# Optimization experiments

Hardware: AMD Instinct MI355X
Metric: run time of the kernel (lower is better)

## Reference

```python
import jax, jax.numpy as jnp
from jax import lax
import numpy as np

V, E, NF = 50000, 300, 1          # vocab, embed_size, n_features
H = 256                            # hidden size (both layers)
B, TH, TB = 128, 32, 512           # batch, headline len, body len
NC = 4                             # n_classes


def setup_inputs() -> dict:
    key = jax.random.key(0)
    ks = jax.random.split(key, 24)
    emb = jax.random.normal(ks[0], (V, E), jnp.float32) * 0.1
    emb = emb.at[0].set(0.0)  # pad token -> zero row so seqlen masking is meaningful

    def make_ids(kid, klen, T):
        raw = jax.random.randint(kid, (B, T, NF), 1, V)
        lens = jax.random.randint(klen, (B,), max(T // 4, 1), T + 1)
        mask = jnp.arange(T)[None, :, None] < lens[:, None, None]
        return jnp.where(mask, raw, 0)

    headline_ids = make_ids(ks[1], ks[2], TH)
    body_ids = make_ids(ks[3], ks[4], TB)

    def gru_params(k, din, h):
        k1, k2 = jax.random.split(k, 2)
        s = 1.0 / np.sqrt(din + h)
        return (jax.random.normal(k1, (din + h, 2 * h), jnp.float32) * s,
                jnp.ones((2 * h,), jnp.float32),          # TF GRUCell gate bias init = 1.0
                jax.random.normal(k2, (din + h, h), jnp.float32) * s,
                jnp.zeros((h,), jnp.float32))

    D0 = NF * E
    hd0 = gru_params(ks[5], D0, H)
    hd1 = gru_params(ks[6], H, H)
    bd0 = gru_params(ks[7], D0, H)
    bd1 = gru_params(ks[8], H, H)

    W_pred = jax.random.normal(ks[9], (2 * H, NC), jnp.float32) * (1.0 / np.sqrt(2 * H))
    b_pred = jnp.zeros((NC,), jnp.float32)

    out = {"headline_ids": headline_ids, "body_ids": body_ids, "embeddings": emb,
           "W_pred": W_pred, "b_pred": b_pred}
    for pref, p in (("hd0", hd0), ("hd1", hd1), ("bd0", bd0), ("bd1", bd1)):
        out[pref + "_Wg"], out[pref + "_bg"], out[pref + "_Wc"], out[pref + "_bc"] = p
    return out


def _seq_length(x):
    # used = sign(max(|x|, axis=2)); seqlen = sum over time
    return jnp.sum(jnp.sign(jnp.max(jnp.abs(x), axis=2)), axis=1).astype(jnp.int32)


def _gru_layer(x, seqlen, Wg, bg, Wc, bc):
    # x: [B, T, D] -> outputs [B, T, H], final state [B, H]; dynamic_rnn semantics:
    # past seqlen, output is zero and state is copied through.
    Bsz, T, _ = x.shape
    Hh = Wc.shape[1]
    xt = jnp.swapaxes(x, 0, 1)  # [T, B, D]
    tids = jnp.arange(T)

    def step(h, inp):
        xi, t = inp
        xh = jnp.concatenate([xi, h], axis=-1)
        r, u = jnp.split(jax.nn.sigmoid(xh @ Wg + bg), 2, axis=-1)
        c = jnp.tanh(jnp.concatenate([xi, r * h], axis=-1) @ Wc + bc)
        nh = u * h + (1.0 - u) * c
        valid = (t < seqlen)[:, None]
        out = jnp.where(valid, nh, 0.0)
        h_next = jnp.where(valid, nh, h)
        return h_next, out

    h0 = jnp.zeros((Bsz, Hh), x.dtype)
    hf, outs = lax.scan(step, h0, (xt, tids))
    return jnp.swapaxes(outs, 0, 1), hf


def _stream(ids, emb, layers):
    x = emb[ids].reshape(ids.shape[0], ids.shape[1], -1)  # [B, T, NF*E]
    h = None
    for (Wg, bg, Wc, bc) in layers:
        sl = _seq_length(x)  # recomputed from current layer inputs, as in the source
        x, h = _gru_layer(x, sl, Wg, bg, Wc, bc)
    return h


def reference(headline_ids, body_ids, embeddings,
              hd0_Wg, hd0_bg, hd0_Wc, hd0_bc, hd1_Wg, hd1_bg, hd1_Wc, hd1_bc,
              bd0_Wg, bd0_bg, bd0_Wc, bd0_bc, bd1_Wg, bd1_bg, bd1_Wc, bd1_bc,
              W_pred, b_pred):
    h_head = _stream(headline_ids, embeddings,
                     [(hd0_Wg, hd0_bg, hd0_Wc, hd0_bc), (hd1_Wg, hd1_bg, hd1_Wc, hd1_bc)])
    h_body = _stream(body_ids, embeddings,
                     [(bd0_Wg, bd0_bg, bd0_Wc, bd0_bc), (bd1_Wg, bd1_bg, bd1_Wc, bd1_bc)])
    pred_input = jnp.concatenate([h_head, h_body], axis=1)  # [B, 2H]
    return pred_input @ W_pred + b_pred                      # [B, NC]
```

## Files before the change

### kernel.cpp

```cpp
#include <hip/hip_runtime.h>
#include <cstdint>
#include <cstddef>

#define H_    256
#define NG    768
#define BATCH 128
#define TH_   32
#define TB_   512
#define E_    300
#define RPB   16
#define CH_   16
#define NCH   32
#define NT_   192
#define RING  4
#define NJ    72
#define NGRU  24
#define NWORK 200
#define GRID  (NGRU + NWORK)

#define G0S   ((size_t)BATCH * CH_ * NG)
#define OCS   ((size_t)BATCH * CH_ * H_)

#define F_QHEAD 0
#define F_CNT0  1
#define F_CNT1  33
#define F_L0F   65
#define F_L1F   97
#define F_HCNT0 129
#define F_HCNT1 131
#define F_HL0F  133
#define F_NUM   136

typedef _Float16 half8 __attribute__((ext_vector_type(8)));
typedef _Float16 half4 __attribute__((ext_vector_type(4)));
typedef float    floatx4 __attribute__((ext_vector_type(4)));

#define AS1 __attribute__((address_space(1)))
#define AS3 __attribute__((address_space(3)))

#define WC_LGKM0 0xC07F
#define WCVM(N)  (0x0F70 | ((N) & 15) | (((N) >> 4) << 14))

__global__ __launch_bounds__(256) void pack_bias(
    const float* __restrict__ bg, const float* __restrict__ bc,
    float* __restrict__ bias)
{
  int idx = blockIdx.x * 256 + threadIdx.x;
  if (idx < NG) bias[idx] = (idx < 2 * H_) ? bg[idx] : bc[idx - 2 * H_];
}

__global__ __launch_bounds__(256) void pack_bx(
    const float* __restrict__ Wg, const float* __restrict__ Wc,
    int din, int KT, _Float16* __restrict__ out)
{
  int idx = blockIdx.x * 256 + threadIdx.x;
  if (idx >= KT * 48 * 64) return;
  int lane = idx & 63, tile = idx >> 6;
  int kt = tile / 48, nt = tile - kt * 48;
  int col = nt * 16 + (lane & 15);
  int k0 = kt * 32 + (lane >> 4) * 8;
  const float* W; int ncols, c2;
  if (col < 2 * H_) { W = Wg; ncols = 2 * H_; c2 = col; }
  else              { W = Wc; ncols = H_;     c2 = col - 2 * H_; }
  _Float16* dst = out + ((size_t)(kt * 48 + nt) * 64 + lane) * 8;
#pragma unroll
  for (int j = 0; j < 8; ++j) {
    int k = k0 + j;
    dst[j] = (k < din) ? (_Float16)W[(size_t)k * ncols + c2] : (_Float16)0.f;
  }
}

__global__ __launch_bounds__(256) void pack_w(
    const float* __restrict__ Wg, const float* __restrict__ Wc, int din,
    _Float16* __restrict__ wpk)
{
  int idx = blockIdx.x * 256 + threadIdx.x;
  if (idx >= 48 * 64) return;
  int tile = idx >> 6, lane = idx & 63;
  int grp = tile >> 4, tt = tile & 15;
  int wv = tt >> 1, s = tt & 1;
  const float* W; int ncols, n0;
  if (grp == 0)      { W = Wg; ncols = 2 * H_; n0 = wv * 32 + s * 16; }
  else if (grp == 1) { W = Wg; ncols = 2 * H_; n0 = 256 + wv * 32 + s * 16; }
  else               { W = Wc; ncols = H_;     n0 = wv * 32 + s * 16; }
  int n = n0 + (lane & 15);
  int kb = (lane >> 4) * 8;
#pragma unroll
  for (int kt = 0; kt < 8; ++kt) {
    _Float16* dst = wpk + ((size_t)(tile * 8 + kt) * 64 + lane) * 8;
#pragma unroll
    for (int j = 0; j < 8; ++j)
      dst[j] = (_Float16)W[(size_t)(din + kt * 32 + kb + j) * ncols + n];
  }
}

__global__ __launch_bounds__(256) void seq_k(const int* __restrict__ ids, int T,
                                             int* __restrict__ seq)
{
  __shared__ int red[256];
  int b = blockIdx.x, tid = threadIdx.x;
  int cnt = 0;
  for (int t = tid; t < T; t += 256) cnt += (ids[b * T + t] != 0) ? 1 : 0;
  red[tid] = cnt;
  __syncthreads();
  for (int s = 128; s > 0; s >>= 1) {
    if (tid < s) red[tid] += red[tid + s];
    __syncthreads();
  }
  if (tid == 0) seq[b] = red[0];
}

struct GemmJob {
  const _Float16* Adir; const int* ids; const _Float16* Bpk;
  const float* bias; _Float16* G;
  int K; int KT; int t0; int tcsh; int T;
};

struct PArgs {
  const float* emb; const int* idsH; const int* idsB;
  const int* seqH; const int* seqB;
  const _Float16 *Wpk0, *Wpk1, *Wpk2, *Wpk3;
  const _Float16 *Bx0, *Bx1, *Bx2, *Bx3;
  const float *bi0, *bi1, *bi2, *bi3;
  _Float16 *G0r, *G1r, *Ocr;
  _Float16 *GH0, *GH1, *OcH;
  float *hfH, *hfB;
  int* flg;
};

union SMem {
  struct { _Float16 hpk[4096]; _Float16 rpk[4096]; _Float16 Gs[4][12288]; } g;
  struct { _Float16 Al[2][64 * 40]; _Float16 Bl[2][8 * 512]; } m;
  int bcast;
};

__device__ __forceinline__ void gemm_block(const GemmJob& jb, const float* emb,
                                           int lb, SMem& sm)
{
  auto& Al = sm.m.Al;
  auto& Bl = sm.m.Bl;
  const int tid = threadIdx.x;
  const int w = tid >> 6, lane = tid & 63;
  const int quad = lane >> 4, l15 = lane & 15;
  const int gx = lb / 6, gy = lb - gx * 6;
  const int m0 = gx * 64, n0 = gy * 128;
  const int K = jb.K, KT = jb.KT, tcsh = jb.tcsh;
  const int tc = 1 << tcsh;

  const int am = tid >> 3, ak = tid & 7;
  const int arow = m0 + am;
  const _Float16* asrch = nullptr;
  const float*    asrcf = nullptr;
  if (jb.Adir) {
    asrch = jb.Adir + (size_t)arow * K;
  } else {
    int b = arow >> tcsh, tl = arow & (tc - 1);
    asrcf = emb + (size_t)jb.ids[b * jb.T + jb.t0 + tl] * K;
  }

  float a4[4];
  auto loadA = [&](int kt) {
    int k0 = kt * 32 + ak * 4;
    if (asrch) {
      half4 hv = *(const half4*)&asrch[k0];
#pragma unroll
      for (int j = 0; j < 4; ++j) a4[j] = (float)hv[j];
    } else {
#pragma unroll
      for (int j = 0; j < 4; ++j) a4[j] = (k0 + j < K) ? asrcf[k0 + j] : 0.f;
    }
  };
  auto writeA = [&](int buf) {
    half4 v;
#pragma unroll
    for (int j = 0; j < 4; ++j) v[j] = (_Float16)a4[j];
    *(half4*)&Al[buf][am * 40 + ak * 4] = v;
  };
  auto stageB = [&](int kt, int buf) {
    int nt = (n0 >> 4) + w;
    const _Float16* src = jb.Bpk + ((size_t)(kt * 48 + nt) * 64 + lane) * 8;
    __builtin_amdgcn_global_load_lds(
        (const AS1 unsigned int*)src,
        (AS3 unsigned int*)&Bl[buf][w * 512 + lane * 8], 16, 0, 0);
  };

  loadA(0);
  stageB(0, 0);
  writeA(0);
  floatx4 acc[4] = {};

  for (int kt = 0; kt < KT; ++kt) {
    const int buf = kt & 1;
    __syncthreads();
    if (kt + 1 < KT) { loadA(kt + 1); stageB(kt + 1, buf ^ 1); }
    half8 bf = *(const half8*)&Bl[buf][w * 512 + lane * 8];
#pragma unroll
    for (int st = 0; st < 4; ++st) {
      half8 af = *(const half8*)&Al[buf][(st * 16 + l15) * 40 + quad * 8];
      acc[st] = __builtin_amdgcn_mfma_f32_16x16x32_f16(af, bf, acc[st], 0, 0, 0);
    }
    if (kt + 1 < KT) writeA(buf ^ 1);
  }

  int col = n0 + w * 16 + l15;
  float bb = jb.bias[col];
  int g = col >> 8, kk = col & 255;
  int ww = kk >> 5, ss = (kk >> 4) & 1, ll = kk & 15;
  int cc = 2 * g + ss;
#pragma unroll
  for (int st = 0; st < 4; ++st) {
#pragma unroll
    for (int r = 0; r < 4; ++r) {
      int grow = m0 + st * 16 + quad * 4 + r;
      int b = grow >> tcsh, tl = grow & (tc - 1);
      int rg = b >> 4, mm = b & 15, qb = mm >> 2, rb = mm & 3;
      jb.G[((size_t)tl * BATCH + rg * RPB) * NG +
           ((ww * 6 + cc) * 64 + qb * 16 + ll) * 4 + rb] =
          (_Float16)(acc[st][r] + bb);
    }
  }
}

struct GruRun {
  const _Float16* W; const int* seq; int rg; int nch;
  const _Float16* Gb; size_t gs; int ring;
  _Float16* Ob; size_t os;
  float* stOut;
  int* wflag; int wtar;
  int* w2flag;
  int* pflag;
};

__device__ __forceinline__ void gru_run(const GruRun& P, SMem& sm)
{
  _Float16* hpk = sm.g.hpk;
  _Float16* rpk = sm.g.rpk;
  auto& Gs = sm.g.Gs;

  const int tid = threadIdx.x;
  const int w = tid >> 6, lane = tid & 63;
  const int quad = lane >> 4, l15 = lane & 15;

  floatx4 wg[4][8];
  floatx4 wc[2][8];
#pragma unroll
  for (int i = 0; i < 4; ++i) {
    const int tile = (i >> 1) * 16 + w * 2 + (i & 1);
#pragma unroll
    for (int kt = 0; kt < 8; ++kt) {
      wg[i][kt] = *(const floatx4*)&P.W[((size_t)(tile * 8 + kt) * 64 + lane) * 8];
      asm volatile("" : "+v"(wg[i][kt]));
    }
  }
#pragma unroll
  for (int i = 0; i < 2; ++i) {
    const int tile = 32 + w * 2 + i;
#pragma unroll
    for (int kt = 0; kt < 8; ++kt) {
      wc[i][kt] = *(const floatx4*)&P.W[((size_t)(tile * 8 + kt) * 64 + lane) * 8];
      asm volatile("" : "+a"(wc[i][kt]));
    }
  }

  int seq4[4];
#pragma unroll
  for (int r = 0; r < 4; ++r) seq4[r] = P.seq[P.rg * RPB + quad * 4 + r];
  int Smax = 0;
#pragma unroll
  for (int i = 0; i < 16; ++i) Smax = max(Smax, P.seq[P.rg * RPB + i]);

  const int wbase = (w * 64 + quad * 2 + (l15 >> 3)) * 8 + (l15 & 7);
  const int rbase = (((quad >> 1) << 5) + ((l15 & 3) << 3) +
                     ((l15 >> 2) << 1) + (quad & 1)) * 8;

  float h_reg[2][4];
#pragma unroll
  for (int s = 0; s < 2; ++s)
#pragma unroll
    for (int r = 0; r < 4; ++r) {
      h_reg[s][r] = 0.f;
      hpk[wbase + s * 256 + r * 64] = (_Float16)0.f;
    }

  const _Float16* hA = &hpk[rbase];
  const _Float16* rA = &rpk[rbase];

  for (int c = 0; c < P.nch; ++c) {
    if (tid == 0) {
      while (__hip_atomic_load(&P.wflag[c], __ATOMIC_RELAXED,
                               __HIP_MEMORY_SCOPE_AGENT) < P.wtar)
        __builtin_amdgcn_s_sleep(2);
      if (P.w2flag && c >= RING)
        while (__hip_atomic_load(&P.w2flag[c - RING], __ATOMIC_RELAXED,
                                 __HIP_MEMORY_SCOPE_AGENT) < NT_)
          __builtin_amdgcn_s_sleep(2);
      __builtin_amdgcn_fence(__ATOMIC_ACQUIRE, "agent");
    }
    __syncthreads();

    const int slot = P.ring ? (c & (RING - 1)) : c;
    const _Float16* G = P.Gb + (size_t)slot * P.gs;
    _Float16* outp = P.Ob ? P.Ob + (size_t)slot * P.os : nullptr;
    const int t0 = c * CH_;
    int steps = Smax - t0;
    if (steps < 0) steps = 0;
    if (steps > CH_) steps = CH_;

    const _Float16* gblk = G + (size_t)P.rg * RPB * NG + w * 1536;
    _Float16* ldsw = &Gs[0][0] + w * 1536;
    auto stage = [&](int t, int buf) {
      const _Float16* gp = gblk + (size_t)t * BATCH * NG;
      _Float16* lp = ldsw + buf * 12288;
#pragma unroll
      for (int i = 0; i < 3; ++i) {
        __builtin_amdgcn_global_load_lds(
            (const AS1 unsigned int*)(gp + i * 512 + lane * 8),
            (AS3 unsigned int*)(lp + i * 512), 16, 0, 0);
      }
    };
    if (steps > 0) stage(0, 0);
    __syncthreads();
    if (steps > 1) stage(1, 1);
    if (steps > 2) stage(2, 2);

    for (int t = 0; t < steps; ++t) {
      const int buf = t & 3;
      if (t + 3 < steps) stage(t + 3, (t + 3) & 3);

      floatx4 acc[4] = {};
#pragma unroll
      for (int kt = 0; kt < 8; ++kt) {
        half8 a = *(const half8*)&hA[kt * 512];
#pragma unroll
        for (int s = 0; s < 4; ++s)
          acc[s] = __builtin_amdgcn_mfma_f32_16x16x32_f16(
              a, __builtin_bit_cast(half8, wg[s][kt]), acc[s], 0, 0, 0);
      }

      {
        int np = outp ? ((t < 3) ? t : 3) : 0;
        int nf = steps - 1 - t; if (nf > 3) nf = 3;
        switch (np * 4 + nf) {
          case  0: __builtin_amdgcn_s_waitcnt(WCVM(0));  break;
          case  1: __builtin_amdgcn_s_waitcnt(WCVM(3));  break;
          case  2: __builtin_amdgcn_s_waitcnt(WCVM(6));  break;
          case  3: __builtin_amdgcn_s_waitcnt(WCVM(9));  break;
          case  4: __builtin_amdgcn_s_waitcnt(WCVM(8));  break;
          case  5: __builtin_amdgcn_s_waitcnt(WCVM(11)); break;
          case  6: __builtin_amdgcn_s_waitcnt(WCVM(14)); break;
          case  7: __builtin_amdgcn_s_waitcnt(WCVM(17)); break;
          case  8: __builtin_amdgcn_s_waitcnt(WCVM(16)); break;
          case  9: __builtin_amdgcn_s_waitcnt(WCVM(19)); break;
          case 10: __builtin_amdgcn_s_waitcnt(WCVM(22)); break;
          case 11: __builtin_amdgcn_s_waitcnt(WCVM(25)); break;
          case 12: __builtin_amdgcn_s_waitcnt(WCVM(24)); break;
          case 13: __builtin_amdgcn_s_waitcnt(WCVM(27)); break;
          case 14: __builtin_amdgcn_s_waitcnt(WCVM(30)); break;
          default: __builtin_amdgcn_s_waitcnt(WCVM(33)); break;
        }
      }

      floatx4 gA[4];
#pragma unroll
      for (int cc = 0; cc < 4; ++cc) {
        half4 hv = *(const half4*)&Gs[buf][(w * 6 + cc) * 256 + lane * 4];
#pragma unroll
        for (int j = 0; j < 4; ++j) gA[cc][j] = (float)hv[j];
      }

#pragma unroll
      for (int s = 0; s < 2; ++s)
#pragma unroll
        for (int r = 0; r < 4; ++r) {
          float pre = acc[s][r] + gA[s][r];
          float g = __builtin_amdgcn_rcpf(1.f + __expf(-pre));
          rpk[wbase + s * 256 + r * 64] = (_Float16)(g * h_reg[s][r]);
        }
      float u_reg[2][4];
#pragma unroll
      for (int s = 0; s < 2; ++s)
#pragma unroll
        for (int r = 0; r < 4; ++r) {
          float pre = acc[2 + s][r] + gA[2 + s][r];
          u_reg[s][r] = __builtin_amdgcn_rcpf(1.f + __expf(-pre));
        }
      __builtin_amdgcn_s_waitcnt(WC_LGKM0);
      __builtin_amdgcn_s_barrier();

      floatx4 accB[2] = {};
#pragma unroll
      for (int kt = 0; kt < 8; ++kt) {
        half8 a = *(const half8*)&rA[kt * 512];
#pragma unroll
        for (int s = 0; s < 2; ++s)
          accB[s] = __builtin_amdgcn_mfma_f32_16x16x32_f16(
              a, __builtin_bit_cast(half8, wc[s][kt]), accB[s], 0, 0, 0);
      }
      floatx4 gB[2];
#pragma unroll
      for (int s = 0; s < 2; ++s) {
        half4 hv = *(const half4*)&Gs[buf][(w * 6 + 4 + s) * 256 + lane * 4];
#pragma unroll
        for (int j = 0; j < 4; ++j) gB[s][j] = (float)hv[j];
      }

#pragma unroll
      for (int s = 0; s < 2; ++s)
#pragma unroll
        for (int r = 0; r < 4; ++r) {
          int row = quad * 4 + r;
          float pre = accB[s][r] + gB[s][r];
          float cv = 1.f - 2.f * __builtin_amdgcn_rcpf(1.f + __expf(2.f * pre));
          float u = u_reg[s][r];
          float hn = u * h_reg[s][r] + (1.f - u) * cv;
          bool valid = (t0 + t) < seq4[r];
          hn = valid ? hn : h_reg[s][r];
          h_reg[s][r] = hn;
          hpk[wbase + s * 256 + r * 64] = (_Float16)hn;
          if (outp)
            outp[((size_t)(P.rg * RPB + row) * CH_ + t) * H_ +
                 (w * 32 + s * 16 + l15)] = (_Float16)(valid ? hn : 0.f);
        }
      __builtin_amdgcn_s_waitcnt(WC_LGKM0);
      __builtin_amdgcn_s_barrier();
    }

    __syncthreads();
    if (P.pflag && tid == 0) {
      __builtin_amdgcn_fence(__ATOMIC_RELEASE, "agent");
      __hip_atomic_fetch_add(&P.pflag[c], 1, __ATOMIC_RELAXED,
                             __HIP_MEMORY_SCOPE_AGENT);
    }
  }

  if (P.stOut) {
#pragma unroll
    for (int s = 0; s < 2; ++s)
#pragma unroll
      for (int r = 0; r < 4; ++r)
        P.stOut[(size_t)(P.rg * RPB + quad * 4 + r) * H_ +
                (w * 32 + s * 16 + l15)] = h_reg[s][r];
  }
}

__device__ __forceinline__ void worker(const PArgs& a, SMem& sm)
{
  int* flg = a.flg;
  for (;;) {
    if (threadIdx.x == 0)
      sm.bcast = __hip_atomic_fetch_add(&flg[F_QHEAD], 1, __ATOMIC_RELAXED,
                                        __HIP_MEMORY_SCOPE_AGENT);
    __syncthreads();
    int tile = sm.bcast;
    __syncthreads();
    if (tile >= NJ * NT_) return;
    int q = tile / NT_, lb = tile - q * NT_;

    GemmJob jb{};
    int* post = nullptr;
    int* d1 = nullptr; int d1t = 0;
    int* d2 = nullptr; int d2t = 0;
    bool skip = false;

    if (q < 4) {
      int c = q;
      jb = {nullptr, a.idsB, a.Bx2, a.bi2, a.G0r + (size_t)(c & 3) * G0S,
            E_, 10, c * CH_, 4, TB_};
      post = &flg[F_CNT0 + c];
    } else if (q < 6) {
      int c = q - 4;
      jb = {nullptr, a.idsH, a.Bx0, a.bi0, a.GH0 + (size_t)c * G0S,
            E_, 10, c * CH_, 4, TH_};
      post = &flg[F_HCNT0 + c];
    } else if (q < 8) {
      int c = q - 6;
      jb = {a.OcH + (size_t)c * OCS, nullptr, a.Bx1, a.bi1,
            a.GH1 + (size_t)c * G0S, H_, 8, 0, 4, TH_};
      d1 = &flg[F_HL0F + c]; d1t = 8;
      post = &flg[F_HCNT1 + c];
    } else {
      int k = (q - 8) >> 1;
      if (((q - 8) & 1) == 0) {
        jb = {a.Ocr + (size_t)(k & 3) * OCS, nullptr, a.Bx3, a.bi3,
              a.G1r + (size_t)(k & 3) * G0S, H_, 8, 0, 4, TB_};
        d1 = &flg[F_L0F + k]; d1t = 8;
        if (k >= RING) { d2 = &flg[F_L1F + (k - RING)]; d2t = 8; }
        post = &flg[F_CNT1 + k];
      } else {
        int c = k + 4;
        if (c >= NCH) skip = true;
        else {
          jb = {nullptr, a.idsB, a.Bx2, a.bi2, a.G0r + (size_t)(c & 3) * G0S,
                E_, 10, c * CH_, 4, TB_};
          d1 = &flg[F_L0F + (c - RING)]; d1t = 8;
          post = &flg[F_CNT0 + c];
        }
      }
    }
    if (skip) continue;

    if (threadIdx.x == 0) {
      if (d1)
        while (__hip_atomic_load(d1, __ATOMIC_RELAXED,
                                 __HIP_MEMORY_SCOPE_AGENT) < d1t)
          __builtin_amdgcn_s_sleep(8);
      if (d2)
        while (__hip_atomic_load(d2, __ATOMIC_RELAXED,
                                 __HIP_MEMORY_SCOPE_AGENT) < d2t)
          __builtin_amdgcn_s_sleep(8);
      __builtin_amdgcn_fence(__ATOMIC_ACQUIRE, "agent");
    }
    __syncthreads();

    gemm_block(jb, a.emb, lb, sm);

    __syncthreads();
    if (threadIdx.x == 0) {
      __builtin_amdgcn_fence(__ATOMIC_RELEASE, "agent");
      __hip_atomic_fetch_add(post, 1, __ATOMIC_RELAXED,
                             __HIP_MEMORY_SCOPE_AGENT);
    }
  }
}

__global__ __launch_bounds__(512, 1) void pers(PArgs a)
{
  __shared__ SMem sm;
  const int bid = blockIdx.x;
  int* flg = a.flg;

  if (bid < 8) {
    GruRun P{a.Wpk2, a.seqB, bid, NCH, a.G0r, G0S, 1,
             a.Ocr, OCS, nullptr,
             &flg[F_CNT0], NT_, &flg[F_CNT1], &flg[F_L0F]};
    gru_run(P, sm);
  } else if (bid < 16) {
    GruRun P{a.Wpk3, a.seqB, bid - 8, NCH, a.G1r, G0S, 1,
             nullptr, 0, a.hfB,
             &flg[F_CNT1], NT_, nullptr, &flg[F_L1F]};
    gru_run(P, sm);
  } else if (bid < NGRU) {
    GruRun P0{a.Wpk0, a.seqH, bid - 16, 2, a.GH0, G0S, 0,
              a.OcH, OCS, nullptr,
              &flg[F_HCNT0], NT_, nullptr, &flg[F_HL0F]};
    gru_run(P0, sm);
    GruRun P1{a.Wpk1, a.seqH, bid - 16, 2, a.GH1, G0S, 0,
              nullptr, 0, a.hfH,
              &flg[F_HCNT1], NT_, nullptr, nullptr};
    gru_run(P1, sm);
  } else {
    worker(a, sm);
  }
}

__global__ __launch_bounds__(512) void pred_k(
    const float* __restrict__ hh, const float* __restrict__ hb,
    const float* __restrict__ Wp, const float* __restrict__ bpred,
    float* __restrict__ out)
{
  int tid = threadIdx.x;
  int b = tid >> 2, c = tid & 3;
  float acc = bpred[c];
  for (int k = 0; k < H_; ++k) acc += hh[b * H_ + k] * Wp[k * 4 + c];
  for (int k = 0; k < H_; ++k) acc += hb[b * H_ + k] * Wp[(H_ + k) * 4 + c];
  out[b * 4 + c] = acc;
}

extern "C" void kernel_launch(void* const* d_in, const int* in_sizes, int n_in,
                              void* d_out, int out_size, void* d_ws, size_t ws_size,
                              hipStream_t stream)
{
  (void)in_sizes; (void)n_in; (void)out_size; (void)ws_size;
  const int*   idsH = (const int*)  d_in[0];
  const int*   idsB = (const int*)  d_in[1];
  const float* emb  = (const float*)d_in[2];
  const float* Wp   = (const float*)d_in[3];
  const float* bp   = (const float*)d_in[4];
  const float* W[4][4];
  for (int s = 0; s < 4; ++s)
    for (int q = 0; q < 4; ++q)
      W[s][q] = (const float*)d_in[5 + s * 4 + q];

  float* wbase = (float*)d_ws;
  size_t off = 0;
  auto alloc = [&](size_t n) {
    float* p = wbase + off; off += (n + 255) & ~(size_t)255; return p;
  };

  int* flg = (int*)alloc(F_NUM);
  int* seqH = (int*)alloc(BATCH);
  int* seqB = (int*)alloc(BATCH);
  float* bi[4]; _Float16* Wpk[4]; _Float16* Bxh[4];
  const int din[4] = {E_, H_, E_, H_};
  const int KT[4]  = {10, 8, 10, 8};
  for (int s = 0; s < 4; ++s) {
    bi[s]  = alloc(NG);
    Wpk[s] = (_Float16*)alloc(48 * 8 * 64 * 8 / 2);
    Bxh[s] = (_Float16*)alloc((size_t)KT[s] * 48 * 64 * 8 / 2);
  }
  float* hfH = alloc((size_t)BATCH * H_);
  float* hfB = alloc((size_t)BATCH * H_);

  _Float16* GH0 = (_Float16*)alloc(2 * G0S / 2);
  _Float16* GH1 = (_Float16*)alloc(2 * G0S / 2);
  _Float16* OcH = (_Float16*)alloc(2 * OCS / 2);
  _Float16* G0r = (_Float16*)alloc(RING * G0S / 2);
  _Float16* G1r = (_Float16*)alloc(RING * G0S / 2);
  _Float16* Ocr = (_Float16*)alloc(RING * OCS / 2);

  hipMemsetAsync(flg, 0, F_NUM * sizeof(int), stream);

  for (int s = 0; s < 4; ++s) {
    pack_bias<<<(NG + 255) / 256, 256, 0, stream>>>(W[s][1], W[s][3], bi[s]);
    pack_w<<<(48 * 64 + 255) / 256, 256, 0, stream>>>(
        W[s][0], W[s][2], din[s], Wpk[s]);
    pack_bx<<<(KT[s] * 48 * 64 + 255) / 256, 256, 0, stream>>>(
        W[s][0], W[s][2], din[s], KT[s], Bxh[s]);
  }
  seq_k<<<BATCH, 256, 0, stream>>>(idsH, TH_, seqH);
  seq_k<<<BATCH, 256, 0, stream>>>(idsB, TB_, seqB);

  PArgs a;
  a.emb = emb; a.idsH = idsH; a.idsB = idsB; a.seqH = seqH; a.seqB = seqB;
  a.Wpk0 = Wpk[0]; a.Wpk1 = Wpk[1]; a.Wpk2 = Wpk[2]; a.Wpk3 = Wpk[3];
  a.Bx0 = Bxh[0]; a.Bx1 = Bxh[1]; a.Bx2 = Bxh[2]; a.Bx3 = Bxh[3];
  a.bi0 = bi[0]; a.bi1 = bi[1]; a.bi2 = bi[2]; a.bi3 = bi[3];
  a.G0r = G0r; a.G1r = G1r; a.Ocr = Ocr;
  a.GH0 = GH0; a.GH1 = GH1; a.OcH = OcH;
  a.hfH = hfH; a.hfB = hfB; a.flg = flg;
  pers<<<GRID, 512, 0, stream>>>(a);

  pred_k<<<1, 512, 0, stream>>>(hfH, hfB, Wp, bp, (float*)d_out);
}
```

Measured before the change: 2.213 ms.

## Use per-row-group dependency flags and restructure GRU step MFMA scheduling

Replaces the per-chunk global counters with per-chunk, per-row-group flags, so each GRU block waits only on the 24 GEMM tiles covering its own 16 batch rows instead of all 192. Pipelines can then advance per row group rather than per whole chunk. The GRU step is also reordered: G-tile reads are hoisted before the next prefetch, gate MFMAs are split so the reset-gate math overlaps the update-gate MFMAs, and the candidate matmul uses split-K accumulators. Per-step validity selects are replaced by a snapshot of the final state at seqlen, which changes the padded-step output semantics. This relies on padded steps being harmless given zero pad embeddings and zero inputs past seqlen.

```diff
diff --git a/kernel.cpp b/kernel.cpp
--- a/kernel.cpp
+++ b/kernel.cpp
@@ -12,6 +12,7 @@
 #define CH_   16
 #define NCH   32
 #define NT_   192
+#define NTRG  24
 #define RING  4
 #define NJ    72
 #define NGRU  24
@@ -23,13 +24,13 @@
 
 #define F_QHEAD 0
 #define F_CNT0  1
-#define F_CNT1  33
-#define F_L0F   65
-#define F_L1F   97
-#define F_HCNT0 129
-#define F_HCNT1 131
-#define F_HL0F  133
-#define F_NUM   136
+#define F_L0F   257
+#define F_CNT1  513
+#define F_L1F   769
+#define F_HCNT0 1025
+#define F_HL0F  1041
+#define F_HCNT1 1057
+#define F_NUM   1073
 
 typedef _Float16 half8 __attribute__((ext_vector_type(8)));
 typedef _Float16 half4 __attribute__((ext_vector_type(4)));
@@ -273,12 +274,13 @@
   const int rbase = (((quad >> 1) << 5) + ((l15 & 3) << 3) +
                      ((l15 >> 2) << 1) + (quad & 1)) * 8;
 
-  float h_reg[2][4];
+  const bool dosnap = (P.stOut != nullptr);
+  float h_reg[2][4], snap[2][4];
 #pragma unroll
   for (int s = 0; s < 2; ++s)
 #pragma unroll
     for (int r = 0; r < 4; ++r) {
-      h_reg[s][r] = 0.f;
+      h_reg[s][r] = 0.f; snap[s][r] = 0.f;
       hpk[wbase + s * 256 + r * 64] = (_Float16)0.f;
     }
 
@@ -287,12 +289,13 @@
 
   for (int c = 0; c < P.nch; ++c) {
     if (tid == 0) {
-      while (__hip_atomic_load(&P.wflag[c], __ATOMIC_RELAXED,
+      while (__hip_atomic_load(&P.wflag[c * 8 + P.rg], __ATOMIC_RELAXED,
                                __HIP_MEMORY_SCOPE_AGENT) < P.wtar)
         __builtin_amdgcn_s_sleep(2);
       if (P.w2flag && c >= RING)
-        while (__hip_atomic_load(&P.w2flag[c - RING], __ATOMIC_RELAXED,
-                                 __HIP_MEMORY_SCOPE_AGENT) < NT_)
+        while (__hip_atomic_load(&P.w2flag[(c - RING) * 8 + P.rg],
+                                 __ATOMIC_RELAXED,
+                                 __HIP_MEMORY_SCOPE_AGENT) < NTRG)
           __builtin_amdgcn_s_sleep(2);
       __builtin_amdgcn_fence(__ATOMIC_ACQUIRE, "agent");
     }
@@ -325,102 +328,116 @@
 
     for (int t = 0; t < steps; ++t) {
       const int buf = t & 3;
-      if (t + 3 < steps) stage(t + 3, (t + 3) & 3);
-
-      floatx4 acc[4] = {};
-#pragma unroll
-      for (int kt = 0; kt < 8; ++kt) {
-        half8 a = *(const half8*)&hA[kt * 512];
-#pragma unroll
-        for (int s = 0; s < 4; ++s)
-          acc[s] = __builtin_amdgcn_mfma_f32_16x16x32_f16(
-              a, __builtin_bit_cast(half8, wg[s][kt]), acc[s], 0, 0, 0);
-      }
 
       {
         int np = outp ? ((t < 3) ? t : 3) : 0;
-        int nf = steps - 1 - t; if (nf > 3) nf = 3;
-        switch (np * 4 + nf) {
+        int nf = steps - 1 - t; if (nf > 2) nf = 2;
+        switch (np * 3 + nf) {
           case  0: __builtin_amdgcn_s_waitcnt(WCVM(0));  break;
           case  1: __builtin_amdgcn_s_waitcnt(WCVM(3));  break;
           case  2: __builtin_amdgcn_s_waitcnt(WCVM(6));  break;
-          case  3: __builtin_amdgcn_s_waitcnt(WCVM(9));  break;
-          case  4: __builtin_amdgcn_s_waitcnt(WCVM(8));  break;
-          case  5: __builtin_amdgcn_s_waitcnt(WCVM(11)); break;
-          case  6: __builtin_amdgcn_s_waitcnt(WCVM(14)); break;
-          case  7: __builtin_amdgcn_s_waitcnt(WCVM(17)); break;
-          case  8: __builtin_amdgcn_s_waitcnt(WCVM(16)); break;
-          case  9: __builtin_amdgcn_s_waitcnt(WCVM(19)); break;
-          case 10: __builtin_amdgcn_s_waitcnt(WCVM(22)); break;
-          case 11: __builtin_amdgcn_s_waitcnt(WCVM(25)); break;
-          case 12: __builtin_amdgcn_s_waitcnt(WCVM(24)); break;
-          case 13: __builtin_amdgcn_s_waitcnt(WCVM(27)); break;
-          case 14: __builtin_amdgcn_s_waitcnt(WCVM(30)); break;
-          default: __builtin_amdgcn_s_waitcnt(WCVM(33)); break;
+          case  3: __builtin_amdgcn_s_waitcnt(WCVM(8));  break;
+          case  4: __builtin_amdgcn_s_waitcnt(WCVM(11)); break;
+          case  5: __builtin_amdgcn_s_waitcnt(WCVM(14)); break;
+          case  6: __builtin_amdgcn_s_waitcnt(WCVM(16)); break;
+          case  7: __builtin_amdgcn_s_waitcnt(WCVM(19)); break;
+          case  8: __builtin_amdgcn_s_waitcnt(WCVM(22)); break;
+          case  9: __builtin_amdgcn_s_waitcnt(WCVM(24)); break;
+          case 10: __builtin_amdgcn_s_waitcnt(WCVM(27)); break;
+          default: __builtin_amdgcn_s_waitcnt(WCVM(30)); break;
         }
       }
 
-      floatx4 gA[4];
-#pragma unroll
-      for (int cc = 0; cc < 4; ++cc) {
-        half4 hv = *(const half4*)&Gs[buf][(w * 6 + cc) * 256 + lane * 4];
-#pragma unroll
-        for (int j = 0; j < 4; ++j) gA[cc][j] = (float)hv[j];
-      }
-
-#pragma unroll
-      for (int s = 0; s < 2; ++s)
-#pragma unroll
-        for (int r = 0; r < 4; ++r) {
-          float pre = acc[s][r] + gA[s][r];
-          float g = __builtin_amdgcn_rcpf(1.f + __expf(-pre));
-          rpk[wbase + s * 256 + r * 64] = (_Float16)(g * h_reg[s][r]);
-        }
-      float u_reg[2][4];
-#pragma unroll
-      for (int s = 0; s < 2; ++s)
-#pragma unroll
-        for (int r = 0; r < 4; ++r) {
-          float pre = acc[2 + s][r] + gA[2 + s][r];
-          u_reg[s][r] = __builtin_amdgcn_rcpf(1.f + __expf(-pre));
-        }
+      half4 hga[6];
+#pragma unroll
+      for (int cc = 0; cc < 6; ++cc)
+        hga[cc] = *(const half4*)&Gs[buf][(w * 6 + cc) * 256 + lane * 4];
+
+      if (t + 3 < steps) stage(t + 3, (t + 3) & 3);
+
+      floatx4 a0 = {}, a1 = {};
+#pragma unroll
+      for (int kt = 0; kt < 8; ++kt) {
+        half8 a = *(const half8*)&hA[kt * 512];
+        a0 = __builtin_amdgcn_mfma_f32_16x16x32_f16(
+            a, __builtin_bit_cast(half8, wg[0][kt]), a0, 0, 0, 0);
+        a1 = __builtin_amdgcn_mfma_f32_16x16x32_f16(
+            a, __builtin_bit_cast(half8, wg[1][kt]), a1, 0, 0, 0);
+      }
+#pragma unroll
+      for (int r = 0; r < 4; ++r) {
+        float pre0 = a0[r] + (float)hga[0][r];
+        float g0 = __builtin_amdgcn_rcpf(1.f + __expf(-pre0));
+        rpk[wbase + 0 * 256 + r * 64] = (_Float16)(g0 * h_reg[0][r]);
+        float pre1 = a1[r] + (float)hga[1][r];
+        float g1 = __builtin_amdgcn_rcpf(1.f + __expf(-pre1));
+        rpk[wbase + 1 * 256 + r * 64] = (_Float16)(g1 * h_reg[1][r]);
+      }
+      floatx4 a2 = {}, a3 = {};
+#pragma unroll
+      for (int kt = 0; kt < 8; ++kt) {
+        half8 a = *(const half8*)&hA[kt * 512];
+        a2 = __builtin_amdgcn_mfma_f32_16x16x32_f16(
+            a, __builtin_bit_cast(half8, wg[2][kt]), a2, 0, 0, 0);
+        a3 = __builtin_amdgcn_mfma_f32_16x16x32_f16(
+            a, __builtin_bit_cast(half8, wg[3][kt]), a3, 0, 0, 0);
+      }
       __builtin_amdgcn_s_waitcnt(WC_LGKM0);
       __builtin_amdgcn_s_barrier();
 
-      floatx4 accB[2] = {};
-#pragma unroll
-      for (int kt = 0; kt < 8; ++kt) {
+      floatx4 c0 = {}, c1 = {}, c2 = {}, c3 = {};
+#pragma unroll
+      for (int kt = 0; kt < 4; ++kt) {
         half8 a = *(const half8*)&rA[kt * 512];
-#pragma unroll
-        for (int s = 0; s < 2; ++s)
-          accB[s] = __builtin_amdgcn_mfma_f32_16x16x32_f16(
-              a, __builtin_bit_cast(half8, wc[s][kt]), accB[s], 0, 0, 0);
-      }
-      floatx4 gB[2];
-#pragma unroll
-      for (int s = 0; s < 2; ++s) {
-        half4 hv = *(const half4*)&Gs[buf][(w * 6 + 4 + s) * 256 + lane * 4];
-#pragma unroll
-        for (int j = 0; j < 4; ++j) gB[s][j] = (float)hv[j];
+        c0 = __builtin_amdgcn_mfma_f32_16x16x32_f16(
+            a, __builtin_bit_cast(half8, wc[0][kt]), c0, 0, 0, 0);
+        c2 = __builtin_amdgcn_mfma_f32_16x16x32_f16(
+            a, __builtin_bit_cast(half8, wc[1][kt]), c2, 0, 0, 0);
+      }
+#pragma unroll
+      for (int kt = 4; kt < 8; ++kt) {
+        half8 a = *(const half8*)&rA[kt * 512];
+        c1 = __builtin_amdgcn_mfma_f32_16x16x32_f16(
+            a, __builtin_bit_cast(half8, wc[0][kt]), c1, 0, 0, 0);
+        c3 = __builtin_amdgcn_mfma_f32_16x16x32_f16(
+            a, __builtin_bit_cast(half8, wc[1][kt]), c3, 0, 0, 0);
+      }
+      float u_reg[2][4];
+#pragma unroll
+      for (int r = 0; r < 4; ++r) {
+        u_reg[0][r] = __builtin_amdgcn_rcpf(
+            1.f + __expf(-(a2[r] + (float)hga[2][r])));
+        u_reg[1][r] = __builtin_amdgcn_rcpf(
+            1.f + __expf(-(a3[r] + (float)hga[3][r])));
       }
 
 #pragma unroll
       for (int s = 0; s < 2; ++s)
 #pragma unroll
         for (int r = 0; r < 4; ++r) {
-          int row = quad * 4 + r;
-          float pre = accB[s][r] + gB[s][r];
+          float pre = (s == 0 ? c0[r] + c1[r] : c2[r] + c3[r]) +
+                      (float)hga[4 + s][r];
           float cv = 1.f - 2.f * __builtin_amdgcn_rcpf(1.f + __expf(2.f * pre));
           float u = u_reg[s][r];
           float hn = u * h_reg[s][r] + (1.f - u) * cv;
-          bool valid = (t0 + t) < seq4[r];
-          hn = valid ? hn : h_reg[s][r];
           h_reg[s][r] = hn;
           hpk[wbase + s * 256 + r * 64] = (_Float16)hn;
-          if (outp)
-            outp[((size_t)(P.rg * RPB + row) * CH_ + t) * H_ +
-                 (w * 32 + s * 16 + l15)] = (_Float16)(valid ? hn : 0.f);
         }
+      if (dosnap) {
+#pragma unroll
+        for (int s = 0; s < 2; ++s)
+#pragma unroll
+          for (int r = 0; r < 4; ++r)
+            snap[s][r] = (t0 + t + 1 == seq4[r]) ? h_reg[s][r] : snap[s][r];
+      }
+      if (outp) {
+#pragma unroll
+        for (int s = 0; s < 2; ++s)
+#pragma unroll
+          for (int r = 0; r < 4; ++r)
+            outp[((size_t)(P.rg * RPB + quad * 4 + r) * CH_ + t) * H_ +
+                 (w * 32 + s * 16 + l15)] = (_Float16)h_reg[s][r];
+      }
       __builtin_amdgcn_s_waitcnt(WC_LGKM0);
       __builtin_amdgcn_s_barrier();
     }
@@ -428,7 +445,7 @@
     __syncthreads();
     if (P.pflag && tid == 0) {
       __builtin_amdgcn_fence(__ATOMIC_RELEASE, "agent");
-      __hip_atomic_fetch_add(&P.pflag[c], 1, __ATOMIC_RELAXED,
+      __hip_atomic_fetch_add(&P.pflag[c * 8 + P.rg], 1, __ATOMIC_RELAXED,
                              __HIP_MEMORY_SCOPE_AGENT);
     }
   }
@@ -439,7 +456,7 @@
 #pragma unroll
       for (int r = 0; r < 4; ++r)
         P.stOut[(size_t)(P.rg * RPB + quad * 4 + r) * H_ +
-                (w * 32 + s * 16 + l15)] = h_reg[s][r];
+                (w * 32 + s * 16 + l15)] = snap[s][r];
   }
 }
 
@@ -455,45 +472,46 @@
     __syncthreads();
     if (tile >= NJ * NT_) return;
     int q = tile / NT_, lb = tile - q * NT_;
+    int rg = (lb / 6) >> 2;
 
     GemmJob jb{};
     int* post = nullptr;
-    int* d1 = nullptr; int d1t = 0;
-    int* d2 = nullptr; int d2t = 0;
+    int* d1 = nullptr;
+    int* d2 = nullptr;
     bool skip = false;
 
     if (q < 4) {
       int c = q;
       jb = {nullptr, a.idsB, a.Bx2, a.bi2, a.G0r + (size_t)(c & 3) * G0S,
             E_, 10, c * CH_, 4, TB_};
-      post = &flg[F_CNT0 + c];
+      post = &flg[F_CNT0 + c * 8 + rg];
     } else if (q < 6) {
       int c = q - 4;
       jb = {nullptr, a.idsH, a.Bx0, a.bi0, a.GH0 + (size_t)c * G0S,
             E_, 10, c * CH_, 4, TH_};
-      post = &flg[F_HCNT0 + c];
+      post = &flg[F_HCNT0 + c * 8 + rg];
     } else if (q < 8) {
       int c = q - 6;
       jb = {a.OcH + (size_t)c * OCS, nullptr, a.Bx1, a.bi1,
             a.GH1 + (size_t)c * G0S, H_, 8, 0, 4, TH_};
-      d1 = &flg[F_HL0F + c]; d1t = 8;
-      post = &flg[F_HCNT1 + c];
+      d1 = &flg[F_HL0F + c * 8 + rg];
+      post = &flg[F_HCNT1 + c * 8 + rg];
     } else {
       int k = (q - 8) >> 1;
       if (((q - 8) & 1) == 0) {
         jb = {a.Ocr + (size_t)(k & 3) * OCS, nullptr, a.Bx3, a.bi3,
               a.G1r + (size_t)(k & 3) * G0S, H_, 8, 0, 4, TB_};
-        d1 = &flg[F_L0F + k]; d1t = 8;
-        if (k >= RING) { d2 = &flg[F_L1F + (k - RING)]; d2t = 8; }
-        post = &flg[F_CNT1 + k];
+        d1 = &flg[F_L0F + k * 8 + rg];
+        if (k >= RING) d2 = &flg[F_L1F + (k - RING) * 8 + rg];
+        post = &flg[F_CNT1 + k * 8 + rg];
       } else {
         int c = k + 4;
         if (c >= NCH) skip = true;
         else {
           jb = {nullptr, a.idsB, a.Bx2, a.bi2, a.G0r + (size_t)(c & 3) * G0S,
                 E_, 10, c * CH_, 4, TB_};
-          d1 = &flg[F_L0F + (c - RING)]; d1t = 8;
-          post = &flg[F_CNT0 + c];
+          d1 = &flg[F_L0F + (c - RING) * 8 + rg];
+          post = &flg[F_CNT0 + c * 8 + rg];
         }
       }
     }
@@ -502,11 +520,11 @@
     if (threadIdx.x == 0) {
       if (d1)
         while (__hip_atomic_load(d1, __ATOMIC_RELAXED,
-                                 __HIP_MEMORY_SCOPE_AGENT) < d1t)
+                                 __HIP_MEMORY_SCOPE_AGENT) < 1)
           __builtin_amdgcn_s_sleep(8);
       if (d2)
         while (__hip_atomic_load(d2, __ATOMIC_RELAXED,
-                                 __HIP_MEMORY_SCOPE_AGENT) < d2t)
+                                 __HIP_MEMORY_SCOPE_AGENT) < 1)
           __builtin_amdgcn_s_sleep(8);
       __builtin_amdgcn_fence(__ATOMIC_ACQUIRE, "agent");
     }
@@ -532,21 +550,21 @@
   if (bid < 8) {
     GruRun P{a.Wpk2, a.seqB, bid, NCH, a.G0r, G0S, 1,
              a.Ocr, OCS, nullptr,
-             &flg[F_CNT0], NT_, &flg[F_CNT1], &flg[F_L0F]};
+             &flg[F_CNT0], NTRG, &flg[F_CNT1], &flg[F_L0F]};
     gru_run(P, sm);
   } else if (bid < 16) {
     GruRun P{a.Wpk3, a.seqB, bid - 8, NCH, a.G1r, G0S, 1,
              nullptr, 0, a.hfB,
-             &flg[F_CNT1], NT_, nullptr, &flg[F_L1F]};
+             &flg[F_CNT1], NTRG, nullptr, &flg[F_L1F]};
     gru_run(P, sm);
   } else if (bid < NGRU) {
     GruRun P0{a.Wpk0, a.seqH, bid - 16, 2, a.GH0, G0S, 0,
               a.OcH, OCS, nullptr,
-              &flg[F_HCNT0], NT_, nullptr, &flg[F_HL0F]};
+              &flg[F_HCNT0], NTRG, nullptr, &flg[F_HL0F]};
     gru_run(P0, sm);
     GruRun P1{a.Wpk1, a.seqH, bid - 16, 2, a.GH1, G0S, 0,
               nullptr, 0, a.hfH,
-              &flg[F_HCNT1], NT_, nullptr, nullptr};
+              &flg[F_HCNT1], NTRG, nullptr, nullptr};
     gru_run(P1, sm);
   } else {
     worker(a, sm);
```

New measurement: 2.124 ms. 4.1% less time.
